# Optimization experiments

Measured on AMD Instinct MI355X. Metric: run time of the kernel, lower is better.

Reference implementation:

```python
import jax, jax.numpy as jnp
import numpy as np

H, FF, E = 1024, 4096, 8
CAP_FACTOR, MIN_CAP = 1.0, 4
B, S = 4, 2048


def setup_inputs() -> dict:
    key = jax.random.key(0)
    ks = jax.random.split(key, 8)
    g = lambda k, shape, sc: jax.random.normal(k, shape, jnp.float32) * sc
    return {
        "hidden_states": jax.random.normal(ks[0], (B, S, H), jnp.float32),
        "wg": g(ks[1], (H, E), 0.02),
        "w1": g(ks[2], (E, H, FF), 0.02),
        "w2": g(ks[3], (E, FF, H), 0.02),
        "res_w1": g(ks[4], (H, FF), 0.02),
        "res_w2": g(ks[5], (FF, H), 0.02),
        "coef_w": g(ks[6], (H, 2), 0.02),
        "coef_b": jnp.zeros((2,), jnp.float32),
    }


def reference(hidden_states, wg, w1, w2, res_w1, res_w2, coef_w, coef_b):
    x = hidden_states
    b, s, d = x.shape
    tokens = x.reshape(-1, d)                      # [s, m] flattened tokens
    n = tokens.shape[0]
    capacity = max(MIN_CAP, int(CAP_FACTOR * n / E))  # static

    # ---- TopKGate (top-1, deterministic, no RTS) ----
    logits = tokens @ wg                            # [s, e]
    gates = jax.nn.softmax(logits, axis=1)
    idx1 = jnp.argmax(gates, axis=1)                # [s]
    mask1 = jax.nn.one_hot(idx1, E, dtype=jnp.int32)  # [s, e]
    exp_counts = mask1.sum(axis=0)                  # [e]
    # load-balancing aux loss (computed pre-capacity-drop, as in DeepSpeed)
    me = gates.mean(axis=0)
    ce = mask1.astype(gates.dtype).mean(axis=0)
    l_aux = jnp.sum(me * ce) * E
    # capacity-based token dropping (position within expert's buffer)
    locations1 = jnp.cumsum(mask1, axis=0) - 1      # [s, e]
    mask1 = mask1 * (locations1 < capacity).astype(jnp.int32)
    loc1_s = jnp.sum(locations1 * mask1, axis=1)    # [s]
    mask1f = mask1.astype(gates.dtype)
    gates_masked = gates * mask1f                   # zero except kept expert
    loc_sc = jax.nn.one_hot(loc1_s, capacity, dtype=gates.dtype)  # [s, c]
    combine = jnp.einsum("se,sc->sec", gates_masked, loc_sc)      # [s, e, c]
    dispatch = (combine > 0).astype(tokens.dtype)                 # [s, e, c]

    # ---- dispatch -> grouped expert FFN -> combine ----
    dispatched = jnp.einsum("sec,sm->ecm", dispatch, tokens)      # [e, c, m]
    h = jax.nn.gelu(jnp.einsum("ecm,emf->ecf", dispatched, w1))
    expert_out = jnp.einsum("ecf,efm->ecm", h, w2)                # [e, c, m]
    moe_out = jnp.einsum("sec,ecm->sm", combine, expert_out).reshape(b, s, d)

    # ---- residual MoE blend ----
    res = jax.nn.gelu(x @ res_w1) @ res_w2
    coef = jax.nn.softmax(x @ coef_w + coef_b, axis=-1)           # [b, s, 2]
    out = moe_out * coef[..., 0:1] + res * coef[..., 1:2]
    return out, l_aux, exp_counts
```

## Files before the change

kernel.cpp:

```cpp
#include <hip/hip_runtime.h>

typedef unsigned short u16;
typedef unsigned int u32;
typedef float f32x4 __attribute__((ext_vector_type(4)));
typedef __bf16 bf16x8 __attribute__((ext_vector_type(8)));

#define NTOK 8192
#define HDIM 1024
#define FFDIM 4096
#define NEXP 8
#define CAP 1024

typedef const __attribute__((address_space(1))) void gvoid_t;
typedef __attribute__((address_space(3))) void lvoid_t;

__device__ __forceinline__ u16 f2bf(float f) {
  u32 u = __float_as_uint(f);
  u += 0x7fffu + ((u >> 16) & 1u);
  return (u16)(u >> 16);
}

__device__ __forceinline__ float gelu_f(float x) {
  float u = 1.5957691216057308f * (x + 0.044715f * x * x * x);
  return x / (1.0f + __expf(-u));
}

__global__ __launch_bounds__(256) void convert_bf16(const float* __restrict__ src,
                                                    u16* __restrict__ dst,
                                                    long long n) {
  long long i = ((long long)blockIdx.x * 256 + threadIdx.x) * 8;
  if (i >= n) return;
  float4 f0 = *(const float4*)(src + i);
  float4 f1 = *(const float4*)(src + i + 4);
  union { u16 u[8]; uint4 v; } o;
  o.u[0] = f2bf(f0.x); o.u[1] = f2bf(f0.y); o.u[2] = f2bf(f0.z); o.u[3] = f2bf(f0.w);
  o.u[4] = f2bf(f1.x); o.u[5] = f2bf(f1.y); o.u[6] = f2bf(f1.z); o.u[7] = f2bf(f1.w);
  *(uint4*)(dst + i) = o.v;
}

__global__ __launch_bounds__(256) void transpose_f32_bf16(const float* __restrict__ src,
                                                          long long sBatch,
                                                          u16* __restrict__ dst,
                                                          long long dBatch,
                                                          int R, int C) {
  __shared__ float tile[32][33];
  int z = blockIdx.z;
  const float* s = src + (long long)z * sBatch;
  u16* d = dst + (long long)z * dBatch;
  int c0 = blockIdx.x * 32, r0 = blockIdx.y * 32;
  int tx = threadIdx.x, ty = threadIdx.y;
#pragma unroll
  for (int i = 0; i < 32; i += 8)
    tile[ty + i][tx] = s[(long long)(r0 + ty + i) * C + c0 + tx];
  __syncthreads();
#pragma unroll
  for (int i = 0; i < 32; i += 8)
    d[(long long)(c0 + ty + i) * R + r0 + tx] = f2bf(tile[tx][ty + i]);
}

__global__ __launch_bounds__(256) void gate_kernel(const float* __restrict__ x,
                                                   const float* __restrict__ wg,
                                                   const float* __restrict__ cw,
                                                   const float* __restrict__ cb,
                                                   int* __restrict__ idx1,
                                                   float* __restrict__ gate_val,
                                                   float* __restrict__ gates8,
                                                   float* __restrict__ coef) {
  const int wave = threadIdx.x >> 6, lane = threadIdx.x & 63;
  const int s = blockIdx.x * 4 + wave;
  const float* xr = x + (long long)s * HDIM;
  double p[10];
#pragma unroll
  for (int v = 0; v < 10; ++v) p[v] = 0.0;
#pragma unroll 4
  for (int i = 0; i < HDIM / 64; ++i) {
    int hh = i * 64 + lane;
    float xv = xr[hh];
    float4 w0 = *(const float4*)(wg + hh * 8);
    float4 w1 = *(const float4*)(wg + hh * 8 + 4);
    float2 c = *(const float2*)(cw + hh * 2);
    double xd = (double)xv;
    p[0] += xd * (double)w0.x; p[1] += xd * (double)w0.y;
    p[2] += xd * (double)w0.z; p[3] += xd * (double)w0.w;
    p[4] += xd * (double)w1.x; p[5] += xd * (double)w1.y;
    p[6] += xd * (double)w1.z; p[7] += xd * (double)w1.w;
    p[8] += xd * (double)c.x;  p[9] += xd * (double)c.y;
  }
#pragma unroll
  for (int v = 0; v < 10; ++v)
#pragma unroll
    for (int off = 32; off > 0; off >>= 1) p[v] += __shfl_down(p[v], off);
  if (lane == 0) {
    double mx = p[0]; int am = 0;
#pragma unroll
    for (int e = 1; e < 8; ++e)
      if (p[e] > mx) { mx = p[e]; am = e; }
    float g[8]; float sum = 0.f;
#pragma unroll
    for (int e = 0; e < 8; ++e) { g[e] = __expf((float)(p[e] - mx)); sum += g[e]; }
    float inv = 1.f / sum;
#pragma unroll
    for (int e = 0; e < 8; ++e) { g[e] *= inv; gates8[s * 8 + e] = g[e]; }
    idx1[s] = am;
    gate_val[s] = g[am];
    float c0 = (float)p[8] + cb[0], c1 = (float)p[9] + cb[1];
    float m2 = fmaxf(c0, c1);
    float e0 = __expf(c0 - m2), e1 = __expf(c1 - m2);
    float is = 1.f / (e0 + e1);
    coef[2 * s] = e0 * is;
    coef[2 * s + 1] = e1 * is;
  }
}

__global__ void scan_kernel(const int* __restrict__ idx1,
                            const float* __restrict__ gates8,
                            int* __restrict__ rowmap,
                            float* __restrict__ out_tail)
{
  int lane = threadIdx.x;
  int cnt[8];
  float me[8];
#pragma unroll
  for (int e = 0; e < 8; ++e) { cnt[e] = 0; me[e] = 0.f; }
  unsigned long long below = (lane == 0) ? 0ull : ((~0ull) >> (64 - lane));
  int eN = idx1[lane];
  float4 gN0 = *(const float4*)(gates8 + lane * 8);
  float4 gN1 = *(const float4*)(gates8 + lane * 8 + 4);
  for (int it = 0; it < NTOK / 64; ++it) {
    int tok = it * 64 + lane;
    int e = eN;
    float4 g0 = gN0, g1 = gN1;
    if (it + 1 < NTOK / 64) {
      eN = idx1[tok + 64];
      gN0 = *(const float4*)(gates8 + (tok + 64) * 8);
      gN1 = *(const float4*)(gates8 + (tok + 64) * 8 + 4);
    }
    me[0] += g0.x; me[1] += g0.y; me[2] += g0.z; me[3] += g0.w;
    me[4] += g1.x; me[5] += g1.y; me[6] += g1.z; me[7] += g1.w;
#pragma unroll
    for (int xx = 0; xx < 8; ++xx) {
      unsigned long long m = __ballot(e == xx);
      if (e == xx) {
        int pos = cnt[xx] + __popcll(m & below);
        if (pos < CAP) rowmap[xx * CAP + pos] = tok;
      }
      cnt[xx] += __popcll(m);
    }
  }
#pragma unroll
  for (int xx = 0; xx < 8; ++xx)
#pragma unroll
    for (int off = 32; off > 0; off >>= 1) me[xx] += __shfl_down(me[xx], off);
  if (lane == 0) {
    float laux = 0.f;
#pragma unroll
    for (int e = 0; e < 8; ++e) {
      out_tail[1 + e] = (float)cnt[e];
      laux += (me[e] / (float)NTOK) * ((float)cnt[e] / (float)NTOK);
    }
    out_tail[0] = laux * (float)NEXP;
  }
}

__global__ __launch_bounds__(256) void gemm128(
    const u16* __restrict__ Aall, long long aBatch,
    const u16* __restrict__ Ball, long long bBatch,
    int M, int N, int K,
    const int* __restrict__ amapAll,
    int mode,
    u16* __restrict__ hOut, long long hBatch,
    const int* __restrict__ rmapAll,
    const float* __restrict__ gate_val,
    float* __restrict__ moe_acc,
    const float* __restrict__ coef,
    float* __restrict__ outf) {
  const int z = blockIdx.z;
  const u16* A = Aall + (long long)z * aBatch;
  const u16* Bt = Ball + (long long)z * bBatch;

  const int tid = threadIdx.x;
  const int lane = tid & 63;
  const int wave = tid >> 6;
  const int wr = wave >> 1, wc = wave & 1;
  const int tileM = blockIdx.y * 128;
  const int tileN = blockIdx.x * 128;

  __shared__ __align__(16) u16 As[128 * 64];
  __shared__ __align__(16) u16 Bs[128 * 64];

  const int lrow = lane >> 3;
  const int gk = (((lane & 7) ^ lrow) << 3);

  int sr[4];
#pragma unroll
  for (int c = 0; c < 4; ++c) sr[c] = wave * 32 + c * 8 + lrow;

  long long gaA[4];
  if (amapAll) {
    const int* amap = amapAll + (long long)z * M;
#pragma unroll
    for (int c = 0; c < 4; ++c) {
      int s0 = amap[tileM + sr[c]];
      gaA[c] = s0 < 0 ? 0 : s0;
    }
  } else {
#pragma unroll
    for (int c = 0; c < 4; ++c) gaA[c] = tileM + sr[c];
  }

  const u16* aG[4];
  const u16* bG[4];
#pragma unroll
  for (int c = 0; c < 4; ++c) {
    aG[c] = A + gaA[c] * K + gk;
    bG[c] = Bt + (long long)(tileN + sr[c]) * K + gk;
  }

  f32x4 acc[4][4];
  const f32x4 fz = {0.f, 0.f, 0.f, 0.f};
#pragma unroll
  for (int i = 0; i < 4; ++i)
#pragma unroll
    for (int j = 0; j < 4; ++j) acc[i][j] = fz;

  const int rlo = lane & 15;
  const int kq = lane >> 4;
  const int sw = rlo & 7;
  const int ks0 = (kq ^ sw) << 3;
  const int ks1 = ((4 | kq) ^ sw) << 3;
  int aRow[4], bRow[4];
#pragma unroll
  for (int i = 0; i < 4; ++i) {
    aRow[i] = (wr * 64 + i * 16 + rlo) * 64;
    bRow[i] = (wc * 64 + i * 16 + rlo) * 64;
  }

  for (int kk = 0; kk < K; kk += 64) {
    __syncthreads();
#pragma unroll
    for (int c = 0; c < 4; ++c) {
      __builtin_amdgcn_global_load_lds((gvoid_t*)aG[c],
          (lvoid_t*)&As[(wave * 32 + c * 8) * 64], 16, 0, 0);
      __builtin_amdgcn_global_load_lds((gvoid_t*)bG[c],
          (lvoid_t*)&Bs[(wave * 32 + c * 8) * 64], 16, 0, 0);
      aG[c] += 64;
      bG[c] += 64;
    }
    __syncthreads();
#pragma unroll
    for (int sub = 0; sub < 2; ++sub) {
      const int ks = sub ? ks1 : ks0;
      bf16x8 af[4], bfr[4];
#pragma unroll
      for (int i = 0; i < 4; ++i) af[i] = *(const bf16x8*)(&As[aRow[i] + ks]);
#pragma unroll
      for (int j = 0; j < 4; ++j) bfr[j] = *(const bf16x8*)(&Bs[bRow[j] + ks]);
#pragma unroll
      for (int i = 0; i < 4; ++i)
#pragma unroll
        for (int j = 0; j < 4; ++j)
          acc[i][j] = __builtin_amdgcn_mfma_f32_16x16x32_bf16(af[i], bfr[j], acc[i][j], 0, 0, 0);
    }
  }

  const int qr = (lane >> 4) * 4;
  const int cc = lane & 15;
  if (mode == 0) {
    u16* hO = hOut + (long long)z * hBatch;
#pragma unroll
    for (int i = 0; i < 4; ++i) {
      int rbase = tileM + wr * 64 + i * 16 + qr;
#pragma unroll
      for (int j = 0; j < 4; ++j) {
        int col = tileN + wc * 64 + j * 16 + cc;
#pragma unroll
        for (int r = 0; r < 4; ++r)
          hO[(long long)(rbase + r) * N + col] = f2bf(gelu_f(acc[i][j][r]));
      }
    }
  } else if (mode == 1) {
    const int* rmap = rmapAll + (long long)z * M;
#pragma unroll
    for (int i = 0; i < 4; ++i) {
      int rbase = tileM + wr * 64 + i * 16 + qr;
#pragma unroll
      for (int j = 0; j < 4; ++j) {
        int col = tileN + wc * 64 + j * 16 + cc;
#pragma unroll
        for (int r = 0; r < 4; ++r) {
          int s = rmap[rbase + r];
          if (s >= 0) moe_acc[(long long)s * HDIM + col] = gate_val[s] * acc[i][j][r];
        }
      }
    }
  } else {
#pragma unroll
    for (int i = 0; i < 4; ++i) {
      int rbase = tileM + wr * 64 + i * 16 + qr;
#pragma unroll
      for (int j = 0; j < 4; ++j) {
        int col = tileN + wc * 64 + j * 16 + cc;
#pragma unroll
        for (int r = 0; r < 4; ++r) {
          int s = rbase + r;
          outf[(long long)s * HDIM + col] =
              coef[2 * s] * moe_acc[(long long)s * HDIM + col] + coef[2 * s + 1] * acc[i][j][r];
        }
      }
    }
  }
}

extern "C" void kernel_launch(void* const* d_in, const int* in_sizes, int n_in,
                              void* d_out, int out_size, void* d_ws, size_t ws_size,
                              hipStream_t stream) {
  (void)in_sizes; (void)n_in; (void)out_size; (void)ws_size;
  const float* x   = (const float*)d_in[0];
  const float* wg  = (const float*)d_in[1];
  const float* w1  = (const float*)d_in[2];
  const float* w2  = (const float*)d_in[3];
  const float* rw1 = (const float*)d_in[4];
  const float* rw2 = (const float*)d_in[5];
  const float* cw  = (const float*)d_in[6];
  const float* cb  = (const float*)d_in[7];
  float* out = (float*)d_out;

  char* ws = (char*)d_ws;
  constexpr size_t OFF_XB   = 0;
  constexpr size_t OFF_W1T  = OFF_XB  + (size_t)NTOK * HDIM * 2;
  constexpr size_t OFF_W2T  = OFF_W1T + (size_t)NEXP * FFDIM * HDIM * 2;
  constexpr size_t OFF_H    = OFF_W2T + (size_t)NEXP * HDIM * FFDIM * 2;
  constexpr size_t OFF_MOE  = OFF_H   + (size_t)NEXP * CAP * FFDIM * 2;
  constexpr size_t OFF_GATE = OFF_MOE + (size_t)NTOK * HDIM * 4;
  constexpr size_t OFF_COEF = OFF_GATE + (size_t)NTOK * 4;
  constexpr size_t OFF_IDX  = OFF_COEF + (size_t)NTOK * 8;
  constexpr size_t OFF_RMAP = OFF_IDX + (size_t)NTOK * 4;
  constexpr size_t OFF_G8   = OFF_RMAP + (size_t)NEXP * CAP * 4;

  u16* xb        = (u16*)(ws + OFF_XB);
  u16* w1t       = (u16*)(ws + OFF_W1T);
  u16* w2t       = (u16*)(ws + OFF_W2T);
  u16* h         = (u16*)(ws + OFF_H);
  float* moe_acc = (float*)(ws + OFF_MOE);
  float* gate_v  = (float*)(ws + OFF_GATE);
  float* coef    = (float*)(ws + OFF_COEF);
  int* idx1      = (int*)(ws + OFF_IDX);
  int* rowmap    = (int*)(ws + OFF_RMAP);
  float* gates8  = (float*)(ws + OFF_G8);

  hipMemsetAsync(rowmap, 0xFF, (size_t)NEXP * CAP * 4, stream);
  hipMemsetAsync(moe_acc, 0, (size_t)NTOK * HDIM * 4, stream);

  convert_bf16<<<4096, 256, 0, stream>>>(x, xb, (long long)NTOK * HDIM);
  gate_kernel<<<NTOK / 4, 256, 0, stream>>>(x, wg, cw, cb, idx1, gate_v, gates8, coef);
  scan_kernel<<<1, 64, 0, stream>>>(idx1, gates8, rowmap, out + (size_t)NTOK * HDIM);

  transpose_f32_bf16<<<dim3(FFDIM / 32, HDIM / 32, NEXP), dim3(32, 8), 0, stream>>>(
      w1, (long long)HDIM * FFDIM, w1t, (long long)FFDIM * HDIM, HDIM, FFDIM);
  transpose_f32_bf16<<<dim3(HDIM / 32, FFDIM / 32, NEXP), dim3(32, 8), 0, stream>>>(
      w2, (long long)FFDIM * HDIM, w2t, (long long)HDIM * FFDIM, FFDIM, HDIM);

  gemm128<<<dim3(FFDIM / 128, CAP / 128, NEXP), 256, 0, stream>>>(
      xb, 0, w1t, (long long)FFDIM * HDIM, CAP, FFDIM, HDIM,
      rowmap, 0, h, (long long)CAP * FFDIM, nullptr, nullptr, nullptr, nullptr, nullptr);
  gemm128<<<dim3(HDIM / 128, CAP / 128, NEXP), 256, 0, stream>>>(
      h, (long long)CAP * FFDIM, w2t, (long long)HDIM * FFDIM, CAP, HDIM, FFDIM,
      nullptr, 1, nullptr, 0, rowmap, gate_v, moe_acc, nullptr, nullptr);

  transpose_f32_bf16<<<dim3(FFDIM / 32, HDIM / 32, 1), dim3(32, 8), 0, stream>>>(
      rw1, 0, w1t, 0, HDIM, FFDIM);
  transpose_f32_bf16<<<dim3(HDIM / 32, FFDIM / 32, 1), dim3(32, 8), 0, stream>>>(
      rw2, 0, w2t, 0, FFDIM, HDIM);

  gemm128<<<dim3(FFDIM / 128, NTOK / 128, 1), 256, 0, stream>>>(
      xb, 0, w1t, 0, NTOK, FFDIM, HDIM,
      nullptr, 0, h, 0, nullptr, nullptr, nullptr, nullptr, nullptr);
  gemm128<<<dim3(HDIM / 128, NTOK / 128, 1), 256, 0, stream>>>(
      h, 0, w2t, 0, NTOK, HDIM, FFDIM,
      nullptr, 2, nullptr, 0, nullptr, nullptr, moe_acc, coef, out);
}
```

Before: 897.4 us.

## Replace 128x128 GEMM with double-buffered 256-wide tile, 8-wave pipelined kernel

```diff
diff --git a/kernel.cpp b/kernel.cpp
--- a/kernel.cpp
+++ b/kernel.cpp
@@ -162,7 +162,14 @@
   }
 }
 
-__global__ __launch_bounds__(256) void gemm128(
+
+#define GLDS(gp, lp) __builtin_amdgcn_global_load_lds((gvoid_t*)(gp), (lvoid_t*)(lp), 16, 0, 0)
+#define WAITV(n) asm volatile("s_waitcnt vmcnt(" #n ")" ::: "memory")
+#define MFMA16(a, b, c) __builtin_amdgcn_mfma_f32_16x16x32_bf16(a, b, c, 0, 0, 0)
+#define SBAR() __builtin_amdgcn_s_barrier()
+
+template <int BM>
+__global__ __launch_bounds__(512, 2) void gemm256(
     const u16* __restrict__ Aall, long long aBatch,
     const u16* __restrict__ Ball, long long bBatch,
     int M, int N, int K,
@@ -174,93 +181,193 @@
     float* __restrict__ moe_acc,
     const float* __restrict__ coef,
     float* __restrict__ outf) {
+  constexpr int MF = BM / 64;
+  constexpr int NGA = BM / 64;
   const int z = blockIdx.z;
   const u16* A = Aall + (long long)z * aBatch;
   const u16* Bt = Ball + (long long)z * bBatch;
-
   const int tid = threadIdx.x;
   const int lane = tid & 63;
-  const int wave = tid >> 6;
-  const int wr = wave >> 1, wc = wave & 1;
-  const int tileM = blockIdx.y * 128;
-  const int tileN = blockIdx.x * 128;
-
-  __shared__ __align__(16) u16 As[128 * 64];
-  __shared__ __align__(16) u16 Bs[128 * 64];
-
-  const int lrow = lane >> 3;
-  const int gk = (((lane & 7) ^ lrow) << 3);
-
-  int sr[4];
-#pragma unroll
-  for (int c = 0; c < 4; ++c) sr[c] = wave * 32 + c * 8 + lrow;
-
-  long long gaA[4];
+  const int wv = tid >> 6;
+  const int wv8 = wv * 8;
+  const int wr = wv >> 2, wc = wv & 3;
+  const int tileM = blockIdx.y * BM;
+  const int tileN = blockIdx.x * 256;
+
+  __shared__ __align__(16) u16 As[2][BM * 64];
+  __shared__ __align__(16) u16 Bs[2][256 * 64];
+
+  const int srow = tid >> 3;
+  const int gkS = (((tid & 7) ^ (srow & 7)) << 3);
+  const u16* aP[NGA];
+  const u16* bP[4];
   if (amapAll) {
     const int* amap = amapAll + (long long)z * M;
 #pragma unroll
-    for (int c = 0; c < 4; ++c) {
-      int s0 = amap[tileM + sr[c]];
-      gaA[c] = s0 < 0 ? 0 : s0;
+    for (int g = 0; g < NGA; ++g) {
+      int s0 = amap[tileM + g * 64 + srow];
+      aP[g] = A + (long long)(s0 < 0 ? 0 : s0) * K + gkS;
     }
   } else {
 #pragma unroll
-    for (int c = 0; c < 4; ++c) gaA[c] = tileM + sr[c];
-  }
-
-  const u16* aG[4];
-  const u16* bG[4];
-#pragma unroll
-  for (int c = 0; c < 4; ++c) {
-    aG[c] = A + gaA[c] * K + gk;
-    bG[c] = Bt + (long long)(tileN + sr[c]) * K + gk;
-  }
-
-  f32x4 acc[4][4];
+    for (int g = 0; g < NGA; ++g)
+      aP[g] = A + (long long)(tileM + g * 64 + srow) * K + gkS;
+  }
+#pragma unroll
+  for (int g = 0; g < 4; ++g)
+    bP[g] = Bt + (long long)(tileN + g * 64 + srow) * K + gkS;
+
+#define STAGE_A(nb, h)                                                    \
+  {                                                                       \
+    if constexpr (BM == 256) {                                            \
+      GLDS(aP[2 * (h)], &As[nb][((2 * (h)) * 64 + wv8) * 64]);            \
+      GLDS(aP[2 * (h) + 1], &As[nb][((2 * (h) + 1) * 64 + wv8) * 64]);    \
+      aP[2 * (h)] += 64;                                                  \
+      aP[2 * (h) + 1] += 64;                                              \
+    } else {                                                              \
+      GLDS(aP[(h)], &As[nb][((h) * 64 + wv8) * 64]);                      \
+      aP[(h)] += 64;                                                      \
+    }                                                                     \
+  }
+#define STAGE_B(nb, h)                                                    \
+  {                                                                       \
+    GLDS(bP[2 * (h)], &Bs[nb][((2 * (h)) * 64 + wv8) * 64]);              \
+    GLDS(bP[2 * (h) + 1], &Bs[nb][((2 * (h) + 1) * 64 + wv8) * 64]);      \
+    bP[2 * (h)] += 64;                                                    \
+    bP[2 * (h) + 1] += 64;                                                \
+  }
+
+  STAGE_A(0, 0);
+  STAGE_B(0, 0);
+  STAGE_B(0, 1);
+  STAGE_A(0, 1);
+  if constexpr (BM == 256) { WAITV(4); } else { WAITV(3); }
+  SBAR();
+
+  const int rlo = lane & 15, kq = lane >> 4;
+  const int sw = rlo & 7;
+  const int ksA = ((kq ^ sw) << 3);
+  const int ksB = (((4 | kq) ^ sw) << 3);
+  int aBase[2], bBase[2];
+#pragma unroll
+  for (int qa = 0; qa < 2; ++qa)
+    aBase[qa] = (qa * (BM / 2) + wr * (BM / 4) + rlo) * 64;
+#pragma unroll
+  for (int qb = 0; qb < 2; ++qb)
+    bBase[qb] = (qb * 128 + wc * 32 + rlo) * 64;
+
+  f32x4 acc[2 * MF][4];
   const f32x4 fz = {0.f, 0.f, 0.f, 0.f};
 #pragma unroll
-  for (int i = 0; i < 4; ++i)
+  for (int i = 0; i < 2 * MF; ++i)
 #pragma unroll
     for (int j = 0; j < 4; ++j) acc[i][j] = fz;
 
-  const int rlo = lane & 15;
-  const int kq = lane >> 4;
-  const int sw = rlo & 7;
-  const int ks0 = (kq ^ sw) << 3;
-  const int ks1 = ((4 | kq) ^ sw) << 3;
-  int aRow[4], bRow[4];
-#pragma unroll
-  for (int i = 0; i < 4; ++i) {
-    aRow[i] = (wr * 64 + i * 16 + rlo) * 64;
-    bRow[i] = (wc * 64 + i * 16 + rlo) * 64;
-  }
-
-  for (int kk = 0; kk < K; kk += 64) {
-    __syncthreads();
-#pragma unroll
-    for (int c = 0; c < 4; ++c) {
-      __builtin_amdgcn_global_load_lds((gvoid_t*)aG[c],
-          (lvoid_t*)&As[(wave * 32 + c * 8) * 64], 16, 0, 0);
-      __builtin_amdgcn_global_load_lds((gvoid_t*)bG[c],
-          (lvoid_t*)&Bs[(wave * 32 + c * 8) * 64], 16, 0, 0);
-      aG[c] += 64;
-      bG[c] += 64;
-    }
-    __syncthreads();
-#pragma unroll
-    for (int sub = 0; sub < 2; ++sub) {
-      const int ks = sub ? ks1 : ks0;
-      bf16x8 af[4], bfr[4];
-#pragma unroll
-      for (int i = 0; i < 4; ++i) af[i] = *(const bf16x8*)(&As[aRow[i] + ks]);
-#pragma unroll
-      for (int j = 0; j < 4; ++j) bfr[j] = *(const bf16x8*)(&Bs[bRow[j] + ks]);
-#pragma unroll
-      for (int i = 0; i < 4; ++i)
-#pragma unroll
-        for (int j = 0; j < 4; ++j)
-          acc[i][j] = __builtin_amdgcn_mfma_f32_16x16x32_bf16(af[i], bfr[j], acc[i][j], 0, 0, 0);
-    }
+  const int NT = K / 64;
+  for (int T = 0; T < NT; ++T) {
+    const int p = T & 1, nb = p ^ 1;
+    const bool pre = (T + 1 < NT);
+    const u16* Ap = As[p];
+    const u16* Bp = Bs[p];
+    bf16x8 af[MF][2], bfr[2][2];
+
+#pragma unroll
+    for (int i = 0; i < MF; ++i) {
+      af[i][0] = *(const bf16x8*)&Ap[aBase[0] + i * 1024 + ksA];
+      af[i][1] = *(const bf16x8*)&Ap[aBase[0] + i * 1024 + ksB];
+    }
+#pragma unroll
+    for (int j = 0; j < 2; ++j) {
+      bfr[j][0] = *(const bf16x8*)&Bp[bBase[0] + j * 1024 + ksA];
+      bfr[j][1] = *(const bf16x8*)&Bp[bBase[0] + j * 1024 + ksB];
+    }
+    if (pre) { STAGE_A(nb, 0); STAGE_B(nb, 0); }
+    SBAR();
+    __builtin_amdgcn_s_setprio(1);
+#pragma unroll
+    for (int i = 0; i < MF; ++i)
+#pragma unroll
+      for (int j = 0; j < 2; ++j) {
+        f32x4 c = acc[i][j];
+        c = MFMA16(af[i][0], bfr[j][0], c);
+        c = MFMA16(af[i][1], bfr[j][1], c);
+        acc[i][j] = c;
+      }
+    __builtin_amdgcn_s_setprio(0);
+    if (pre) {
+      if constexpr (BM == 256) { WAITV(6); } else { WAITV(4); }
+    } else { WAITV(0); }
+    SBAR();
+
+#pragma unroll
+    for (int j = 0; j < 2; ++j) {
+      bfr[j][0] = *(const bf16x8*)&Bp[bBase[1] + j * 1024 + ksA];
+      bfr[j][1] = *(const bf16x8*)&Bp[bBase[1] + j * 1024 + ksB];
+    }
+    if (pre) { STAGE_B(nb, 1); }
+    SBAR();
+    __builtin_amdgcn_s_setprio(1);
+#pragma unroll
+    for (int i = 0; i < MF; ++i)
+#pragma unroll
+      for (int j = 0; j < 2; ++j) {
+        f32x4 c = acc[i][2 + j];
+        c = MFMA16(af[i][0], bfr[j][0], c);
+        c = MFMA16(af[i][1], bfr[j][1], c);
+        acc[i][2 + j] = c;
+      }
+    __builtin_amdgcn_s_setprio(0);
+    if (pre) {
+      if constexpr (BM == 256) { WAITV(6); } else { WAITV(5); }
+    } else { WAITV(0); }
+    SBAR();
+
+#pragma unroll
+    for (int i = 0; i < MF; ++i) {
+      af[i][0] = *(const bf16x8*)&Ap[aBase[1] + i * 1024 + ksA];
+      af[i][1] = *(const bf16x8*)&Ap[aBase[1] + i * 1024 + ksB];
+    }
+#pragma unroll
+    for (int j = 0; j < 2; ++j) {
+      bfr[j][0] = *(const bf16x8*)&Bp[bBase[0] + j * 1024 + ksA];
+      bfr[j][1] = *(const bf16x8*)&Bp[bBase[0] + j * 1024 + ksB];
+    }
+    if (pre) { STAGE_A(nb, 1); }
+    SBAR();
+    __builtin_amdgcn_s_setprio(1);
+#pragma unroll
+    for (int i = 0; i < MF; ++i)
+#pragma unroll
+      for (int j = 0; j < 2; ++j) {
+        f32x4 c = acc[MF + i][j];
+        c = MFMA16(af[i][0], bfr[j][0], c);
+        c = MFMA16(af[i][1], bfr[j][1], c);
+        acc[MF + i][j] = c;
+      }
+    __builtin_amdgcn_s_setprio(0);
+    SBAR();
+
+#pragma unroll
+    for (int j = 0; j < 2; ++j) {
+      bfr[j][0] = *(const bf16x8*)&Bp[bBase[1] + j * 1024 + ksA];
+      bfr[j][1] = *(const bf16x8*)&Bp[bBase[1] + j * 1024 + ksB];
+    }
+    SBAR();
+    __builtin_amdgcn_s_setprio(1);
+#pragma unroll
+    for (int i = 0; i < MF; ++i)
+#pragma unroll
+      for (int j = 0; j < 2; ++j) {
+        f32x4 c = acc[MF + i][2 + j];
+        c = MFMA16(af[i][0], bfr[j][0], c);
+        c = MFMA16(af[i][1], bfr[j][1], c);
+        acc[MF + i][2 + j] = c;
+      }
+    __builtin_amdgcn_s_setprio(0);
+    if (pre) {
+      if constexpr (BM == 256) { WAITV(4); } else { WAITV(3); }
+    } else { WAITV(0); }
+    SBAR();
   }
 
   const int qr = (lane >> 4) * 4;
@@ -268,48 +375,66 @@
   if (mode == 0) {
     u16* hO = hOut + (long long)z * hBatch;
 #pragma unroll
-    for (int i = 0; i < 4; ++i) {
-      int rbase = tileM + wr * 64 + i * 16 + qr;
-#pragma unroll
-      for (int j = 0; j < 4; ++j) {
-        int col = tileN + wc * 64 + j * 16 + cc;
-#pragma unroll
-        for (int r = 0; r < 4; ++r)
-          hO[(long long)(rbase + r) * N + col] = f2bf(gelu_f(acc[i][j][r]));
-      }
-    }
+    for (int qa = 0; qa < 2; ++qa)
+#pragma unroll
+      for (int i = 0; i < MF; ++i) {
+        int rbase = tileM + qa * (BM / 2) + wr * (BM / 4) + i * 16 + qr;
+#pragma unroll
+        for (int qb = 0; qb < 2; ++qb)
+#pragma unroll
+          for (int j = 0; j < 2; ++j) {
+            int col = tileN + qb * 128 + wc * 32 + j * 16 + cc;
+#pragma unroll
+            for (int r = 0; r < 4; ++r)
+              hO[(long long)(rbase + r) * N + col] =
+                  f2bf(gelu_f(acc[qa * MF + i][qb * 2 + j][r]));
+          }
+      }
   } else if (mode == 1) {
     const int* rmap = rmapAll + (long long)z * M;
 #pragma unroll
-    for (int i = 0; i < 4; ++i) {
-      int rbase = tileM + wr * 64 + i * 16 + qr;
-#pragma unroll
-      for (int j = 0; j < 4; ++j) {
-        int col = tileN + wc * 64 + j * 16 + cc;
-#pragma unroll
-        for (int r = 0; r < 4; ++r) {
-          int s = rmap[rbase + r];
-          if (s >= 0) moe_acc[(long long)s * HDIM + col] = gate_val[s] * acc[i][j][r];
-        }
-      }
-    }
+    for (int qa = 0; qa < 2; ++qa)
+#pragma unroll
+      for (int i = 0; i < MF; ++i) {
+        int rbase = tileM + qa * (BM / 2) + wr * (BM / 4) + i * 16 + qr;
+#pragma unroll
+        for (int qb = 0; qb < 2; ++qb)
+#pragma unroll
+          for (int j = 0; j < 2; ++j) {
+            int col = tileN + qb * 128 + wc * 32 + j * 16 + cc;
+#pragma unroll
+            for (int r = 0; r < 4; ++r) {
+              int s = rmap[rbase + r];
+              if (s >= 0)
+                moe_acc[(long long)s * HDIM + col] =
+                    gate_val[s] * acc[qa * MF + i][qb * 2 + j][r];
+            }
+          }
+      }
   } else {
 #pragma unroll
-    for (int i = 0; i < 4; ++i) {
-      int rbase = tileM + wr * 64 + i * 16 + qr;
-#pragma unroll
-      for (int j = 0; j < 4; ++j) {
-        int col = tileN + wc * 64 + j * 16 + cc;
-#pragma unroll
-        for (int r = 0; r < 4; ++r) {
-          int s = rbase + r;
-          outf[(long long)s * HDIM + col] =
-              coef[2 * s] * moe_acc[(long long)s * HDIM + col] + coef[2 * s + 1] * acc[i][j][r];
-        }
-      }
-    }
-  }
-}
+    for (int qa = 0; qa < 2; ++qa)
+#pragma unroll
+      for (int i = 0; i < MF; ++i) {
+        int rbase = tileM + qa * (BM / 2) + wr * (BM / 4) + i * 16 + qr;
+#pragma unroll
+        for (int qb = 0; qb < 2; ++qb)
+#pragma unroll
+          for (int j = 0; j < 2; ++j) {
+            int col = tileN + qb * 128 + wc * 32 + j * 16 + cc;
+#pragma unroll
+            for (int r = 0; r < 4; ++r) {
+              int s = rbase + r;
+              outf[(long long)s * HDIM + col] =
+                  coef[2 * s] * moe_acc[(long long)s * HDIM + col] +
+                  coef[2 * s + 1] * acc[qa * MF + i][qb * 2 + j][r];
+            }
+          }
+      }
+  }
+}
+#undef STAGE_A
+#undef STAGE_B
 
 extern "C" void kernel_launch(void* const* d_in, const int* in_sizes, int n_in,
                               void* d_out, int out_size, void* d_ws, size_t ws_size,
@@ -360,10 +485,10 @@
   transpose_f32_bf16<<<dim3(HDIM / 32, FFDIM / 32, NEXP), dim3(32, 8), 0, stream>>>(
       w2, (long long)FFDIM * HDIM, w2t, (long long)HDIM * FFDIM, FFDIM, HDIM);
 
-  gemm128<<<dim3(FFDIM / 128, CAP / 128, NEXP), 256, 0, stream>>>(
+  gemm256<256><<<dim3(FFDIM / 256, CAP / 256, NEXP), 512, 0, stream>>>(
       xb, 0, w1t, (long long)FFDIM * HDIM, CAP, FFDIM, HDIM,
       rowmap, 0, h, (long long)CAP * FFDIM, nullptr, nullptr, nullptr, nullptr, nullptr);
-  gemm128<<<dim3(HDIM / 128, CAP / 128, NEXP), 256, 0, stream>>>(
+  gemm256<128><<<dim3(HDIM / 256, CAP / 128, NEXP), 512, 0, stream>>>(
       h, (long long)CAP * FFDIM, w2t, (long long)HDIM * FFDIM, CAP, HDIM, FFDIM,
       nullptr, 1, nullptr, 0, rowmap, gate_v, moe_acc, nullptr, nullptr);
 
@@ -372,10 +497,10 @@
   transpose_f32_bf16<<<dim3(HDIM / 32, FFDIM / 32, 1), dim3(32, 8), 0, stream>>>(
       rw2, 0, w2t, 0, FFDIM, HDIM);
 
-  gemm128<<<dim3(FFDIM / 128, NTOK / 128, 1), 256, 0, stream>>>(
+  gemm256<256><<<dim3(FFDIM / 256, NTOK / 256, 1), 512, 0, stream>>>(
       xb, 0, w1t, 0, NTOK, FFDIM, HDIM,
       nullptr, 0, h, 0, nullptr, nullptr, nullptr, nullptr, nullptr);
-  gemm128<<<dim3(HDIM / 128, NTOK / 128, 1), 256, 0, stream>>>(
+  gemm256<128><<<dim3(HDIM / 256, NTOK / 128, 1), 512, 0, stream>>>(
       h, 0, w2t, 0, NTOK, HDIM, FFDIM,
       nullptr, 2, nullptr, 0, nullptr, nullptr, moe_acc, coef, out);
 }
```

Result: faster. 870.9 us (-3.0%).
